# Performance work log

Hardware: AMD Instinct MI355X
Metric: run time of the kernel (lower is better)

Reference implementation:

```python
import jax, jax.numpy as jnp
import numpy as np

B, TIN, IN, TRI, D, FFN, L, OUT = 8, 1040, 80, 128, 512, 2048, 8, 1024
H, DH, STRIDE, SEG, RC, LC, MAXMEM = 8, 64, 4, 16, 4, 32, 4
NEG = -1e8
SCALE = DH ** -0.5


def _layer_norm(x, g, b, eps=1e-5):
    m = jnp.mean(x, -1, keepdims=True)
    v = jnp.var(x, -1, keepdims=True)
    return (x - m) * jax.lax.rsqrt(v + eps) * g + b


def _build_attention_mask(U, nseg):
    # Faithful port of Emformer._gen_attention_mask; True = masked out.
    rct = RC * nseg
    mlen = nseg - 1
    rc_rows, q_rows, s_rows = [], [], []
    for i in range(nseg):
        rs, re = i * RC, i * RC + RC
        ss, se = max(i * SEG - LC, 0), min((i + 1) * SEG, U)
        ms = max(i - MAXMEM, 0)
        widths = [ms, i - ms, mlen - i, rs, RC, rct - re, ss, se - ss, U - se]

        def row(allowed):
            return np.concatenate([np.full(max(w, 0), j in allowed, dtype=bool)
                                   for j, w in enumerate(widths)])

        r = row({1, 4, 7})  # memory, own rc block, own (left-extended) segment
        rc_rows.append(np.tile(r, (RC, 1)))
        q_rows.append(np.tile(r, (min(SEG, U - i * SEG), 1)))
        s_rows.append(row({4, 7})[None])  # summary: rc block + segment only
    allow = np.concatenate([np.concatenate(rc_rows), np.concatenate(q_rows), np.concatenate(s_rows)])
    return jnp.asarray(~allow)


def _forward(input, lengths, w_in, ln_in_g, ln_in_b, wq, bq, wk, bk, wv, bv, wo, bo,
             ff_ln_g, ff_ln_b, w1, b1, w2, b2, ln_out_g, ln_out_b, w_out, b_out, lng, lnb):
    x = input @ w_in                                    # (B, TIN, TRI) input_linear (no bias)
    nb, t, _ = x.shape
    nf = t - t % STRIDE
    x = x[:, :nf].reshape(nb, nf // STRIDE, TRI * STRIDE)  # time reduction -> (B, Tr, D)
    lr = lengths // STRIDE
    x = jnp.transpose(x, (1, 0, 2))                     # (Tr, B, D) time-major like torch Emformer
    Tr = x.shape[0]
    U = Tr - RC                                         # utterance length (256)
    nseg = -(-U // SEG)
    utt = x[:U]
    # right-context blocks: hard-copied per segment (last block = trailing rc)
    starts = np.concatenate([np.arange(1, nseg) * SEG, [Tr - RC]])
    idx = (starts[:, None] + np.arange(RC)[None, :]).reshape(-1)
    rc = x[idx]                                         # (nseg*RC, B, D)
    Rt = rc.shape[0]
    Q = Rt + U + nseg                                   # rc + utterance + summary queries
    K = (nseg - 1) + Rt + U                             # mems + rc + utterance keys
    attn_mask = _build_attention_mask(U, nseg)          # (Q, K)
    mems0 = utt.reshape(nseg, SEG, nb, D).mean(1)[:-1]  # AvgPool1d(seg) on raw utterance, drop last
    # padding mask over keys (faithful to _gen_padding_mask)
    rcbl = Q - jnp.max(lr) - nseg
    klen = lr + (nseg - 1) + rcbl
    pad = jnp.arange(K)[None, :] >= klen[:, None]       # (B, K), True = masked

    def step(carry, p):
        utt, rc, mems = carry
        g1, be1, Wq, Bq, Wk, Bk, Wv, Bv, Wo, Bo, g2, be2, Wf1, Bf1, Wf2, Bf2, g3, be3 = p
        ln = _layer_norm(jnp.concatenate([rc, utt]), g1, be1)
        ln_rc, ln_utt = ln[:Rt], ln[Rt:]
        summary = ln_utt.reshape(nseg, SEG, nb, D).mean(1)       # (nseg, B, D)
        qin = jnp.concatenate([ln_rc, ln_utt, summary])          # (Q, B, D)
        kin = jnp.concatenate([mems, ln_rc, ln_utt])             # (K, B, D)
        q = (qin @ Wq + Bq).reshape(Q, nb, H, DH)
        k = (kin @ Wk + Bk).reshape(K, nb, H, DH)
        v = (kin @ Wv + Bv).reshape(K, nb, H, DH)
        w = jnp.einsum('qbhd,kbhd->bhqk', q * SCALE, k)
        w = jnp.where(attn_mask[None, None], NEG, w)
        w = jnp.where(pad[:, None, None, :], NEG, w)
        probs = jax.nn.softmax(w, axis=-1)
        att = jnp.einsum('bhqk,kbhd->qbhd', probs, v).reshape(Q, nb, D)
        out = att @ Wo + Bo
        rcu = out[:Rt + U]
        new_mems = jnp.tanh(out[Rt + U:])[:-1]                   # tanh_on_mem=True, drop last summary
        res = rcu + jnp.concatenate([rc, utt])                   # residual w/ pre-LN input
        h = _layer_norm(res, g2, be2)
        h = jax.nn.relu(h @ Wf1 + Bf1) @ Wf2 + Bf2               # pos_ff (pre-LN inside)
        res = res + h
        res = _layer_norm(res, g3, be3)
        return (res[Rt:], res[:Rt], new_mems), None

    xs = (ln_in_g, ln_in_b, wq, bq, wk, bk, wv, bv, wo, bo,
          ff_ln_g, ff_ln_b, w1, b1, w2, b2, ln_out_g, ln_out_b)
    (utt, rc, mems), _ = jax.lax.scan(step, (utt, rc, mems0), xs)
    y = jnp.transpose(utt, (1, 0, 2))                   # (B, U, D)
    y = _layer_norm(y @ w_out + b_out, lng, lnb)        # output_linear + LayerNorm
    return y, lr


def setup_inputs() -> dict:
    key = jax.random.key(0)
    ks = jax.random.split(key, 12)

    def w(k, shape, fan):
        return jax.random.normal(k, shape, jnp.float32) / np.sqrt(fan)

    return {
        "input": jax.random.normal(ks[0], (B, TIN, IN), jnp.float32),
        "lengths": jax.random.randint(ks[1], (B,), 256, 1025, jnp.int32),
        "w_in": w(ks[2], (IN, TRI), IN),
        "ln_in_g": jnp.ones((L, D), jnp.float32), "ln_in_b": jnp.zeros((L, D), jnp.float32),
        "wq": w(ks[3], (L, D, D), D), "bq": jnp.zeros((L, D), jnp.float32),
        "wk": w(ks[4], (L, D, D), D), "bk": jnp.zeros((L, D), jnp.float32),
        "wv": w(ks[5], (L, D, D), D), "bv": jnp.zeros((L, D), jnp.float32),
        "wo": w(ks[6], (L, D, D), D), "bo": jnp.zeros((L, D), jnp.float32),
        "ff_ln_g": jnp.ones((L, D), jnp.float32), "ff_ln_b": jnp.zeros((L, D), jnp.float32),
        "w1": w(ks[7], (L, D, FFN), D), "b1": jnp.zeros((L, FFN), jnp.float32),
        "w2": w(ks[8], (L, FFN, D), FFN), "b2": jnp.zeros((L, D), jnp.float32),
        "ln_out_g": jnp.ones((L, D), jnp.float32), "ln_out_b": jnp.zeros((L, D), jnp.float32),
        "w_out": w(ks[9], (D, OUT), D), "b_out": jnp.zeros((OUT,), jnp.float32),
        "lng": jnp.ones((OUT,), jnp.float32), "lnb": jnp.zeros((OUT,), jnp.float32),
    }


def reference(input, lengths, w_in, ln_in_g, ln_in_b, wq, bq, wk, bk, wv, bv, wo, bo,
              ff_ln_g, ff_ln_b, w1, b1, w2, b2, ln_out_g, ln_out_b, w_out, b_out, lng, lnb):
    return _forward(input, lengths, w_in, ln_in_g, ln_in_b, wq, bq, wk, bk, wv, bv, wo, bo,
                    ff_ln_g, ff_ln_b, w1, b1, w2, b2, ln_out_g, ln_out_b, w_out, b_out, lng, lnb)
```

## Files before the change

### kernel.cpp

```cpp
#include <hip/hip_runtime.h>
#include <math.h>

#define NB 8
#define D 512
#define H 8
#define DH 64
#define NSEG 16
#define RT 64
#define UU 256
#define QN 336
#define KN 335
#define SROWS 320
#define FFN_D 2048
#define LAYERS 8
#define OUTD 1024
#define TR 260
#define NEGV (-100000000.0f)
#define QSCALE 0.125f

typedef __attribute__((ext_vector_type(8))) short bf16x8;
typedef __attribute__((ext_vector_type(4))) float f32x4;

__device__ inline unsigned short f2bf(float f) {
    union { float f; unsigned int u; } v; v.f = f;
    unsigned int u = v.u;
    unsigned int r = (u + 0x7FFFu + ((u >> 16) & 1u)) >> 16;
    return (unsigned short)r;
}
__device__ inline float bf2f(unsigned short h) {
    union { unsigned int u; float f; } v; v.u = ((unsigned int)h) << 16;
    return v.f;
}

__device__ inline void async16(const void* g, void* l) {
    __builtin_amdgcn_global_load_lds((const __attribute__((address_space(1))) void*)g,
                                     (__attribute__((address_space(3))) void*)l, 16, 0, 0);
}

__global__ void lr_k(const int* __restrict__ lengths, int* __restrict__ lrw,
                     float* __restrict__ out_lr) {
    if (threadIdx.x == 0) {
        int mx = 0;
        for (int b = 0; b < NB; ++b) {
            int v = lengths[b] >> 2;
            lrw[b] = v;
            out_lr[b] = (float)v;
            if (v > mx) mx = v;
        }
        lrw[NB] = mx;
    }
}

__global__ __launch_bounds__(128) void inproj_k(const float* __restrict__ input,
                                                const float* __restrict__ w_in,
                                                float* __restrict__ XB) {
    __shared__ float wl[80 * 128];
    __shared__ float il[4 * 80];
    int tid = threadIdx.x;
    int t = blockIdx.x >> 3;
    int b = blockIdx.x & 7;
    for (int i = tid; i < 80 * 128; i += 128) wl[i] = w_in[i];
    const float* inp = input + ((size_t)b * 1040 + (size_t)t * 4) * 80;
    for (int i = tid; i < 320; i += 128) il[i] = inp[i];
    __syncthreads();
    float* xrow = XB + ((size_t)(t * NB + b)) * D;
#pragma unroll
    for (int c = 0; c < 4; ++c) {
        float acc = 0.f;
        for (int i = 0; i < 80; ++i) acc = fmaf(il[c * 80 + i], wl[i * 128 + tid], acc);
        xrow[c * 128 + tid] = acc;
    }
}

__global__ __launch_bounds__(256) void initstate_k(const float* __restrict__ XB,
                                                   float* __restrict__ S) {
    int r = blockIdx.x;
    int srow = r >> 3, b = r & 7;
    int src;
    if (srow < RT) {
        int i = srow >> 2, jj = srow & 3;
        src = (i < 15 ? (i + 1) * 16 : 256) + jj;
    } else {
        src = srow - RT;
    }
    const float* xr = XB + ((size_t)(src * NB + b)) * D;
    float* sr = S + (size_t)r * D;
    sr[threadIdx.x] = xr[threadIdx.x];
    sr[threadIdx.x + 256] = xr[threadIdx.x + 256];
}

__global__ __launch_bounds__(256) void mems0_k(const float* __restrict__ XB,
                                               unsigned short* __restrict__ MEMS) {
    int ib = blockIdx.x;
    int i = ib >> 3, b = ib & 7;
    for (int c = 0; c < 2; ++c) {
        int col = threadIdx.x + c * 256;
        float s = 0.f;
#pragma unroll
        for (int t = 0; t < 16; ++t) s += XB[((size_t)((i * 16 + t) * NB + b)) * D + col];
        MEMS[(size_t)ib * D + col] = f2bf(s * (1.f / 16.f));
    }
}

__global__ __launch_bounds__(256) void ln2_k(float* __restrict__ X,
                                             unsigned short* __restrict__ Y16,
                                             const float* __restrict__ gA,
                                             const float* __restrict__ bA,
                                             const float* __restrict__ gB,
                                             const float* __restrict__ bB, int fused) {
    int row = blockIdx.x;
    float* x = X + (size_t)row * D;
    __shared__ float rs_[4], rss_[4], rs2[4], rss2[4];
    int w = threadIdx.x >> 6;
    float v[2];
    float s = 0.f, ss = 0.f;
#pragma unroll
    for (int j = 0; j < 2; ++j) {
        v[j] = x[threadIdx.x + j * 256];
        s += v[j];
        ss = fmaf(v[j], v[j], ss);
    }
#pragma unroll
    for (int off = 32; off; off >>= 1) {
        s += __shfl_xor(s, off);
        ss += __shfl_xor(ss, off);
    }
    if ((threadIdx.x & 63) == 0) { rs_[w] = s; rss_[w] = ss; }
    __syncthreads();
    s = rs_[0] + rs_[1] + rs_[2] + rs_[3];
    ss = rss_[0] + rss_[1] + rss_[2] + rss_[3];
    float mean = s * (1.f / D);
    float var = ss * (1.f / D) - mean * mean;
    float rstd = rsqrtf(var + 1e-5f);
    float y1[2];
#pragma unroll
    for (int j = 0; j < 2; ++j) {
        int col = threadIdx.x + j * 256;
        y1[j] = (v[j] - mean) * rstd * gA[col] + bA[col];
    }
    if (!fused) {
#pragma unroll
        for (int j = 0; j < 2; ++j)
            Y16[(size_t)row * D + threadIdx.x + j * 256] = f2bf(y1[j]);
        return;
    }
    float s2 = 0.f, ss2 = 0.f;
#pragma unroll
    for (int j = 0; j < 2; ++j) {
        s2 += y1[j];
        ss2 = fmaf(y1[j], y1[j], ss2);
    }
#pragma unroll
    for (int off = 32; off; off >>= 1) {
        s2 += __shfl_xor(s2, off);
        ss2 += __shfl_xor(ss2, off);
    }
    if ((threadIdx.x & 63) == 0) { rs2[w] = s2; rss2[w] = ss2; }
    __syncthreads();
    s2 = rs2[0] + rs2[1] + rs2[2] + rs2[3];
    ss2 = rss2[0] + rss2[1] + rss2[2] + rss2[3];
    float mean2 = s2 * (1.f / D);
    float var2 = ss2 * (1.f / D) - mean2 * mean2;
    float rstd2 = rsqrtf(var2 + 1e-5f);
#pragma unroll
    for (int j = 0; j < 2; ++j) {
        int col = threadIdx.x + j * 256;
        x[col] = y1[j];
        Y16[(size_t)row * D + col] = f2bf((y1[j] - mean2) * rstd2 * gB[col] + bB[col]);
    }
}

__global__ __launch_bounds__(256) void ln_res_k(const float* __restrict__ OUTB,
                                                float* __restrict__ SB,
                                                unsigned short* __restrict__ MEMS,
                                                unsigned short* __restrict__ Y16,
                                                const float* __restrict__ g,
                                                const float* __restrict__ be) {
    int row = blockIdx.x;
    if (row >= SROWS * NB) {
        int j = row - SROWS * NB;
#pragma unroll
        for (int c = 0; c < 2; ++c) {
            int col = threadIdx.x + c * 256;
            MEMS[(size_t)j * D + col] = f2bf(tanhf(OUTB[(size_t)row * D + col]));
        }
        return;
    }
    float v[2];
    float s = 0.f, ss = 0.f;
#pragma unroll
    for (int j = 0; j < 2; ++j) {
        int col = threadIdx.x + j * 256;
        float r = SB[(size_t)row * D + col] + OUTB[(size_t)row * D + col];
        SB[(size_t)row * D + col] = r;
        v[j] = r;
        s += r;
        ss = fmaf(r, r, ss);
    }
#pragma unroll
    for (int off = 32; off; off >>= 1) {
        s += __shfl_xor(s, off);
        ss += __shfl_xor(ss, off);
    }
    __shared__ float rs_[4], rss_[4];
    int w = threadIdx.x >> 6;
    if ((threadIdx.x & 63) == 0) {
        rs_[w] = s;
        rss_[w] = ss;
    }
    __syncthreads();
    s = rs_[0] + rs_[1] + rs_[2] + rs_[3];
    ss = rss_[0] + rss_[1] + rss_[2] + rss_[3];
    float mean = s * (1.f / D);
    float var = ss * (1.f / D) - mean * mean;
    float rstd = rsqrtf(var + 1e-5f);
#pragma unroll
    for (int j = 0; j < 2; ++j) {
        int col = threadIdx.x + j * 256;
        Y16[(size_t)row * D + col] = f2bf((v[j] - mean) * rstd * g[col] + be[col]);
    }
}

__device__ inline void conv_tile64(float (*tile)[65], const float* __restrict__ src, int srcN,
                                   int k0, int sn0, unsigned short* __restrict__ dst, int dstK,
                                   int dn0) {
    int t = threadIdx.x;
#pragma unroll
    for (int p = 0; p < 4; ++p) {
        int r = p * 16 + (t >> 4);
        int c = (t & 15) * 4;
        *(float4*)&tile[r][c] = *(const float4*)&src[(size_t)(k0 + r) * srcN + sn0 + c];
    }
    __syncthreads();
#pragma unroll
    for (int p = 0; p < 2; ++p) {
        int rn = p * 32 + (t >> 3);
        int kc = (t & 7) * 8;
        int4 o;
        o.x = (int)f2bf(tile[kc + 0][rn]) | ((int)f2bf(tile[kc + 1][rn]) << 16);
        o.y = (int)f2bf(tile[kc + 2][rn]) | ((int)f2bf(tile[kc + 3][rn]) << 16);
        o.z = (int)f2bf(tile[kc + 4][rn]) | ((int)f2bf(tile[kc + 5][rn]) << 16);
        o.w = (int)f2bf(tile[kc + 6][rn]) | ((int)f2bf(tile[kc + 7][rn]) << 16);
        *(int4*)&dst[(size_t)(dn0 + rn) * dstK + k0 + kc] = o;
    }
    __syncthreads();
}

__global__ __launch_bounds__(256) void convw_all_k(const float* __restrict__ wq,
                                                   const float* __restrict__ wk,
                                                   const float* __restrict__ wv,
                                                   const float* __restrict__ wo,
                                                   const float* __restrict__ w1,
                                                   const float* __restrict__ w2,
                                                   const float* __restrict__ bq,
                                                   const float* __restrict__ bk,
                                                   const float* __restrict__ bv,
                                                   const float* __restrict__ w_out,
                                                   unsigned short* __restrict__ WQKV,
                                                   unsigned short* __restrict__ WO16,
                                                   unsigned short* __restrict__ W1T,
                                                   unsigned short* __restrict__ W2T,
                                                   unsigned short* __restrict__ WOUT16,
                                                   float* __restrict__ BQKV) {
    __shared__ float tile[64][65];
    int tb = blockIdx.x;
    if (tb >= LAYERS * 768) {
        int t = tb - LAYERS * 768;
        int n0 = (t % 16) * 64, k0 = (t / 16) * 64;
        conv_tile64(tile, w_out, 1024, k0, n0, WOUT16, 512, n0);
        return;
    }
    int l = tb / 768, t = tb % 768;
    if (t == 0) {
        for (int i = threadIdx.x; i < 1536; i += 256)
            BQKV[l * 1536 + i] = i < 512 ? bq[l * 512 + i]
                                         : (i < 1024 ? bk[l * 512 + i - 512]
                                                     : bv[l * 512 + i - 1024]);
    }
    if (t < 192) {
        int n0 = (t % 24) * 64, k0 = (t / 24) * 64;
        const float* src;
        int sn0;
        if (n0 < 512) { src = wq + (size_t)l * 262144; sn0 = n0; }
        else if (n0 < 1024) { src = wk + (size_t)l * 262144; sn0 = n0 - 512; }
        else { src = wv + (size_t)l * 262144; sn0 = n0 - 1024; }
        conv_tile64(tile, src, 512, k0, sn0, WQKV + (size_t)l * 1536 * 512, 512, n0);
    } else if (t < 256) {
        int tt = t - 192;
        int n0 = (tt % 8) * 64, k0 = (tt / 8) * 64;
        conv_tile64(tile, wo + (size_t)l * 262144, 512, k0, n0, WO16 + (size_t)l * 512 * 512, 512,
                    n0);
    } else if (t < 512) {
        int tt = t - 256;
        int n0 = (tt % 32) * 64, k0 = (tt / 32) * 64;
        conv_tile64(tile, w1 + (size_t)l * 1048576, 2048, k0, n0, W1T + (size_t)l * 2048 * 512,
                    512, n0);
    } else {
        int tt = t - 512;
        int n0 = (tt % 8) * 64, k0 = (tt / 8) * 64;
        conv_tile64(tile, w2 + (size_t)l * 1048576, 512, k0, n0, W2T + (size_t)l * 512 * 2048,
                    2048, n0);
    }
}

__global__ __launch_bounds__(256) void gemm16_k(const unsigned short* __restrict__ A,
                                                const unsigned short* __restrict__ BT,
                                                const float* __restrict__ bias,
                                                void* __restrict__ Cp, int M, int N, int K,
                                                int Kchunk, int flags) {
    __shared__ unsigned short As[2 * 64 * 64];
    __shared__ unsigned short Bs[2 * 64 * 64];
    int tid = threadIdx.x;
    int wave = tid >> 6, lane = tid & 63;
    int wm = wave >> 1, wn = wave & 1;
    int quad = lane >> 4, sub = lane & 15;
    int m0 = blockIdx.y * 64, n0 = blockIdx.x * 64;
    int kb = blockIdx.z * Kchunk;

    int s0 = wave * 128 + lane;
    int s1 = s0 + 64;
    int r0 = s0 >> 3, c0 = (s0 & 7) ^ (r0 & 7);
    int r1 = s1 >> 3, c1 = (s1 & 7) ^ (r1 & 7);
    int gra0 = m0 + r0; if (gra0 >= M) gra0 = M - 1;
    int gra1 = m0 + r1; if (gra1 >= M) gra1 = M - 1;
    const unsigned short* gA0 = A + (size_t)gra0 * K + kb + c0 * 8;
    const unsigned short* gA1 = A + (size_t)gra1 * K + kb + c1 * 8;
    const unsigned short* gB0 = BT + (size_t)(n0 + r0) * K + kb + c0 * 8;
    const unsigned short* gB1 = BT + (size_t)(n0 + r1) * K + kb + c1 * 8;
    int lo0 = (wave * 128) * 8;
    int lo1 = (wave * 128 + 64) * 8;

    int rowA0 = wm * 32 + sub, rowA1 = rowA0 + 16;
    int rowB0 = wn * 32 + sub, rowB1 = rowB0 + 16;

    int nIter = Kchunk >> 6;
    f32x4 acc[2][2] = {};

    async16(gA0, &As[lo0]);
    async16(gA1, &As[lo1]);
    async16(gB0, &Bs[lo0]);
    async16(gB1, &Bs[lo1]);

    for (int it = 0; it < nIter; ++it) {
        __syncthreads();
        int bo = (it & 1) * 4096;
        if (it + 1 < nIter) {
            int nb = ((it + 1) & 1) * 4096;
            int ko = (it + 1) * 64;
            async16(gA0 + ko, &As[nb + lo0]);
            async16(gA1 + ko, &As[nb + lo1]);
            async16(gB0 + ko, &Bs[nb + lo0]);
            async16(gB1 + ko, &Bs[nb + lo1]);
        }
#pragma unroll
        for (int ks = 0; ks < 2; ++ks) {
            int cc = ks * 4 + quad;
            bf16x8 af0 = *(const bf16x8*)&As[bo + rowA0 * 64 + ((cc ^ (rowA0 & 7)) * 8)];
            bf16x8 af1 = *(const bf16x8*)&As[bo + rowA1 * 64 + ((cc ^ (rowA1 & 7)) * 8)];
            bf16x8 bf0 = *(const bf16x8*)&Bs[bo + rowB0 * 64 + ((cc ^ (rowB0 & 7)) * 8)];
            bf16x8 bf1 = *(const bf16x8*)&Bs[bo + rowB1 * 64 + ((cc ^ (rowB1 & 7)) * 8)];
            acc[0][0] = __builtin_amdgcn_mfma_f32_16x16x32_bf16(af0, bf0, acc[0][0], 0, 0, 0);
            acc[0][1] = __builtin_amdgcn_mfma_f32_16x16x32_bf16(af0, bf1, acc[0][1], 0, 0, 0);
            acc[1][0] = __builtin_amdgcn_mfma_f32_16x16x32_bf16(af1, bf0, acc[1][0], 0, 0, 0);
            acc[1][1] = __builtin_amdgcn_mfma_f32_16x16x32_bf16(af1, bf1, acc[1][1], 0, 0, 0);
        }
    }

    bool relu = flags & 1, addc = flags & 2, obf = flags & 4, atom = flags & 8;
    bool addbias = !atom || blockIdx.z == 0;
    float* Cf = (float*)Cp;
    unsigned short* Ch = (unsigned short*)Cp;
#pragma unroll
    for (int mi = 0; mi < 2; ++mi) {
#pragma unroll
        for (int ni = 0; ni < 2; ++ni) {
#pragma unroll
            for (int r = 0; r < 4; ++r) {
                int row = m0 + wm * 32 + mi * 16 + quad * 4 + r;
                int col = n0 + wn * 32 + ni * 16 + sub;
                if (row < M) {
                    float v = acc[mi][ni][r] + (addbias ? bias[col] : 0.f);
                    if (relu) v = fmaxf(v, 0.f);
                    size_t idx = (size_t)row * N + col;
                    if (obf) {
                        Ch[idx] = f2bf(v);
                    } else if (atom) {
                        atomicAdd(&Cf[idx], v);
                    } else {
                        if (addc) v += Cf[idx];
                        Cf[idx] = v;
                    }
                }
            }
        }
    }
}

__global__ __launch_bounds__(256) void attn_k(const unsigned short* __restrict__ QKV,
                                              unsigned short* __restrict__ ATT,
                                              const int* __restrict__ lrw) {
    int tid = threadIdx.x;
    int qrow = blockIdx.x;
    int b = blockIdx.y;

    int i, is_sum;
    if (qrow < RT) {
        i = qrow >> 2;
        is_sum = 0;
    } else if (qrow < RT + UU) {
        i = (qrow - RT) >> 4;
        is_sum = 0;
    } else {
        i = qrow - (RT + UU);
        is_sum = 1;
    }
    int ms = (i > 4) ? (i - 4) : 0;
    int n_mem = is_sum ? 0 : (i - ms);
    int us = (i * 16 - 32 > 0) ? (i * 16 - 32) : 0;
    int ue = (i + 1) * 16;
    int total = n_mem + 4 + (ue - us);
    int klen = KN + lrw[b] - lrw[NB];

    __shared__ float qs[512];
    __shared__ float sc[H][64];
    __shared__ int kks[64];

    if (!is_sum) {
        const unsigned int* qrp =
            (const unsigned int*)&QKV[(size_t)(120 + qrow * NB + b) * 1536];
        unsigned int u = qrp[tid];
        qs[2 * tid] = __uint_as_float(u << 16) * QSCALE;
        qs[2 * tid + 1] = __uint_as_float(u & 0xFFFF0000u) * QSCALE;
    } else {
        const unsigned int* qrp =
            (const unsigned int*)&QKV[(size_t)(120 + (RT + i * 16) * NB + b) * 1536];
        float a0 = 0.f, a1 = 0.f;
#pragma unroll
        for (int t = 0; t < 16; ++t) {
            unsigned int u = qrp[(size_t)t * (NB * 768) + tid];
            a0 += __uint_as_float(u << 16);
            a1 += __uint_as_float(u & 0xFFFF0000u);
        }
        qs[2 * tid] = a0 * (QSCALE / 16.f);
        qs[2 * tid + 1] = a1 * (QSCALE / 16.f);
    }
    if (tid < 64) {
        int kk = -1;
        if (tid < total) {
            if (tid < n_mem)
                kk = ms + tid;
            else if (tid < n_mem + 4)
                kk = 15 + i * 4 + (tid - n_mem);
            else
                kk = 79 + us + (tid - n_mem - 4);
        }
        kks[tid] = kk;
    }
    __syncthreads();

#pragma unroll
    for (int rep = 0; rep < 2; ++rep) {
        int p = rep * 256 + tid;
        int h = p >> 6, j = p & 63;
        int kk = kks[j];
        float s = NEGV;
        if (kk >= 0 && kk < klen) {
            const int4* kr = (const int4*)&QKV[(size_t)(kk * NB + b) * 1536 + 512 + h * DH];
            const float* qh = &qs[h * DH];
            float accd = 0.f;
#pragma unroll
            for (int c = 0; c < 8; ++c) {
                int4 kv = kr[c];
                const int uu[4] = {kv.x, kv.y, kv.z, kv.w};
#pragma unroll
                for (int jj = 0; jj < 4; ++jj) {
                    float lo = __uint_as_float(((unsigned)uu[jj]) << 16);
                    float hi = __uint_as_float(((unsigned)uu[jj]) & 0xFFFF0000u);
                    accd = fmaf(lo, qh[c * 8 + jj * 2], accd);
                    accd = fmaf(hi, qh[c * 8 + jj * 2 + 1], accd);
                }
            }
            s = accd;
        }
        sc[h][j] = s;
    }
    __syncthreads();

    {
        int wv = tid >> 6, lane = tid & 63;
#pragma unroll
        for (int hh = 0; hh < 2; ++hh) {
            int h = wv + hh * 4;
            float s = sc[h][lane];
            float m = s;
#pragma unroll
            for (int off = 32; off; off >>= 1) m = fmaxf(m, __shfl_xor(m, off));
            float p = __expf(s - m);
            float sum = p;
#pragma unroll
            for (int off = 32; off; off >>= 1) sum += __shfl_xor(sum, off);
            sc[h][lane] = p / sum;
        }
    }
    __syncthreads();

    {
        int h = tid >> 5;
        const float* ph = sc[h];
        float a0 = 0.f, a1 = 0.f;
        const unsigned short* vbase = QKV + (size_t)b * 1536 + 1024 + 2 * tid;
#pragma unroll 4
        for (int j = 0; j < total; ++j) {
            int kkj = kks[j];
            unsigned int u = *(const unsigned int*)&vbase[(size_t)kkj * (NB * 1536)];
            float p = ph[j];
            a0 = fmaf(p, __uint_as_float(u << 16), a0);
            a1 = fmaf(p, __uint_as_float(u & 0xFFFF0000u), a1);
        }
        unsigned int o = ((unsigned int)f2bf(a0)) | (((unsigned int)f2bf(a1)) << 16);
        *(unsigned int*)&ATT[(size_t)(qrow * NB + b) * D + 2 * tid] = o;
    }
}

__global__ __launch_bounds__(256) void final_ln_k(const float* __restrict__ Yb,
                                                  const float* __restrict__ g,
                                                  const float* __restrict__ be,
                                                  float* __restrict__ out) {
    int row = blockIdx.x;
    int u = row >> 3, b = row & 7;
    const float* x = Yb + (size_t)row * OUTD;
    float v[4];
    float s = 0.f, ss = 0.f;
#pragma unroll
    for (int j = 0; j < 4; ++j) {
        v[j] = x[threadIdx.x + j * 256];
        s += v[j];
        ss = fmaf(v[j], v[j], ss);
    }
#pragma unroll
    for (int off = 32; off; off >>= 1) {
        s += __shfl_xor(s, off);
        ss += __shfl_xor(ss, off);
    }
    __shared__ float rs_[4], rss_[4];
    int w = threadIdx.x >> 6;
    if ((threadIdx.x & 63) == 0) {
        rs_[w] = s;
        rss_[w] = ss;
    }
    __syncthreads();
    s = rs_[0] + rs_[1] + rs_[2] + rs_[3];
    ss = rss_[0] + rss_[1] + rss_[2] + rss_[3];
    float mean = s * (1.f / OUTD);
    float var = ss * (1.f / OUTD) - mean * mean;
    float rstd = rsqrtf(var + 1e-5f);
    float* o = out + ((size_t)(b * 256 + u)) * OUTD;
#pragma unroll
    for (int j = 0; j < 4; ++j) {
        int col = threadIdx.x + j * 256;
        o[col] = (v[j] - mean) * rstd * g[col] + be[col];
    }
}

extern "C" void kernel_launch(void* const* d_in, const int* in_sizes, int n_in, void* d_out,
                              int out_size, void* d_ws, size_t ws_size, hipStream_t stream) {
    (void)in_sizes;
    (void)n_in;
    (void)out_size;
    (void)ws_size;
    const float* input = (const float*)d_in[0];
    const int* lengths = (const int*)d_in[1];
    const float* w_in = (const float*)d_in[2];
    const float* ln_in_g = (const float*)d_in[3];
    const float* ln_in_b = (const float*)d_in[4];
    const float* wq = (const float*)d_in[5];
    const float* bq = (const float*)d_in[6];
    const float* wk = (const float*)d_in[7];
    const float* bk = (const float*)d_in[8];
    const float* wv = (const float*)d_in[9];
    const float* bv = (const float*)d_in[10];
    const float* wo = (const float*)d_in[11];
    const float* bo = (const float*)d_in[12];
    const float* ff_g = (const float*)d_in[13];
    const float* ff_b = (const float*)d_in[14];
    const float* w1 = (const float*)d_in[15];
    const float* b1 = (const float*)d_in[16];
    const float* w2 = (const float*)d_in[17];
    const float* b2 = (const float*)d_in[18];
    const float* lo_g = (const float*)d_in[19];
    const float* lo_b = (const float*)d_in[20];
    const float* w_out = (const float*)d_in[21];
    const float* b_out = (const float*)d_in[22];
    const float* lng = (const float*)d_in[23];
    const float* lnb = (const float*)d_in[24];
    float* out = (float*)d_out;

    char* wsc = (char*)d_ws;
    size_t off = 0;
    auto alloc = [&](size_t bytes) {
        char* p = wsc + off;
        off += (bytes + 255) & ~(size_t)255;
        return p;
    };
    unsigned short* ACT16 = (unsigned short*)alloc(2688ULL * 512 * 2);
    unsigned short* ATT16 = (unsigned short*)alloc(2688ULL * 512 * 2);
    unsigned short* HB16 = (unsigned short*)alloc(2560ULL * 2048 * 2);
    unsigned short* QKVB = (unsigned short*)alloc(2688ULL * 1536 * 2);
    float* SB = (float*)alloc(2560ULL * 512 * 4);
    unsigned short* WQKV16 = (unsigned short*)alloc(8ULL * 1536 * 512 * 2);
    unsigned short* WO16 = (unsigned short*)alloc(8ULL * 512 * 512 * 2);
    unsigned short* W1T = (unsigned short*)alloc(8ULL * 2048 * 512 * 2);
    unsigned short* W2T = (unsigned short*)alloc(8ULL * 512 * 2048 * 2);
    unsigned short* WOUT16 = (unsigned short*)alloc(1024ULL * 512 * 2);
    float* BQKV = (float*)alloc(8ULL * 1536 * 4);
    int* LRW = (int*)alloc(64);

    unsigned short* MEMS16 = ACT16;
    unsigned short* LNB16 = ACT16 + 120 * 512;
    float* XB = (float*)QKVB;
    float* OUTB = (float*)QKVB;
    float* HBf = (float*)QKVB;

    lr_k<<<1, 64, 0, stream>>>(lengths, LRW, out + (size_t)NB * 256 * 1024);
    convw_all_k<<<LAYERS * 768 + 128, 256, 0, stream>>>(wq, wk, wv, wo, w1, w2, bq, bk, bv,
                                                        w_out, WQKV16, WO16, W1T, W2T, WOUT16,
                                                        BQKV);
    inproj_k<<<TR * NB, 128, 0, stream>>>(input, w_in, XB);
    initstate_k<<<SROWS * NB, 256, 0, stream>>>(XB, SB);
    mems0_k<<<15 * NB, 256, 0, stream>>>(XB, MEMS16);

    for (int l = 0; l < LAYERS; ++l) {
        if (l == 0) {
            ln2_k<<<SROWS * NB, 256, 0, stream>>>(SB, LNB16, ln_in_g, ln_in_b, nullptr, nullptr,
                                                  0);
        } else {
            ln2_k<<<SROWS * NB, 256, 0, stream>>>(SB, LNB16, lo_g + (l - 1) * D,
                                                  lo_b + (l - 1) * D, ln_in_g + l * D,
                                                  ln_in_b + l * D, 1);
        }
        gemm16_k<<<dim3(24, 42, 1), 256, 0, stream>>>(ACT16, WQKV16 + (size_t)l * 1536 * 512,
                                                      BQKV + l * 1536, QKVB, 2680, 1536, 512,
                                                      512, 4);
        attn_k<<<dim3(QN, NB), 256, 0, stream>>>(QKVB, ATT16, LRW);
        gemm16_k<<<dim3(8, 42, 1), 256, 0, stream>>>(ATT16, WO16 + (size_t)l * 512 * 512,
                                                     bo + l * D, OUTB, QN * NB, D, D, 512, 0);
        ln_res_k<<<(SROWS + 15) * NB, 256, 0, stream>>>(OUTB, SB, MEMS16, LNB16, ff_g + l * D,
                                                        ff_b + l * D);
        gemm16_k<<<dim3(32, 40, 1), 256, 0, stream>>>(LNB16, W1T + (size_t)l * 2048 * 512,
                                                      b1 + l * FFN_D, HB16, SROWS * NB, FFN_D,
                                                      512, 512, 1 | 4);
        gemm16_k<<<dim3(8, 40, 4), 256, 0, stream>>>(HB16, W2T + (size_t)l * 512 * 2048,
                                                     b2 + l * D, SB, SROWS * NB, D, FFN_D, 512,
                                                     8);
    }
    ln2_k<<<SROWS * NB, 256, 0, stream>>>(SB, LNB16, lo_g + 7 * D, lo_b + 7 * D, nullptr,
                                          nullptr, 0);
    gemm16_k<<<dim3(16, 32, 1), 256, 0, stream>>>(LNB16 + (size_t)RT * NB * D, WOUT16, b_out,
                                                  HBf, UU * NB, OUTD, 512, 512, 0);
    final_ln_k<<<UU * NB, 256, 0, stream>>>(HBf, lng, lnb, out);
}
```

Measured before the change: 1.176 ms.

## Merge setup kernels and drop GEMM LDS double buffering

Folds the lengths kernel into the weight-conversion launch as one extra block, and merges the initial-state copy and the memory-average kernels into a single launch, removing two kernel launches. The GEMM also goes from double-buffered to single-buffered LDS, issuing its async loads at the top of each K step with a barrier before and after compute. This halves the GEMM's shared memory, which may allow more resident blocks, but it gives up the overlap between the next tile's loads and the current MFMAs.

```diff
diff --git a/kernel.cpp b/kernel.cpp
--- a/kernel.cpp
+++ b/kernel.cpp
@@ -37,20 +37,6 @@
                                      (__attribute__((address_space(3))) void*)l, 16, 0, 0);
 }
 
-__global__ void lr_k(const int* __restrict__ lengths, int* __restrict__ lrw,
-                     float* __restrict__ out_lr) {
-    if (threadIdx.x == 0) {
-        int mx = 0;
-        for (int b = 0; b < NB; ++b) {
-            int v = lengths[b] >> 2;
-            lrw[b] = v;
-            out_lr[b] = (float)v;
-            if (v > mx) mx = v;
-        }
-        lrw[NB] = mx;
-    }
-}
-
 __global__ __launch_bounds__(128) void inproj_k(const float* __restrict__ input,
                                                 const float* __restrict__ w_in,
                                                 float* __restrict__ XB) {
@@ -72,26 +58,26 @@
     }
 }
 
-__global__ __launch_bounds__(256) void initstate_k(const float* __restrict__ XB,
-                                                   float* __restrict__ S) {
+__global__ __launch_bounds__(256) void init2_k(const float* __restrict__ XB,
+                                               float* __restrict__ S,
+                                               unsigned short* __restrict__ MEMS) {
     int r = blockIdx.x;
-    int srow = r >> 3, b = r & 7;
-    int src;
-    if (srow < RT) {
-        int i = srow >> 2, jj = srow & 3;
-        src = (i < 15 ? (i + 1) * 16 : 256) + jj;
-    } else {
-        src = srow - RT;
-    }
-    const float* xr = XB + ((size_t)(src * NB + b)) * D;
-    float* sr = S + (size_t)r * D;
-    sr[threadIdx.x] = xr[threadIdx.x];
-    sr[threadIdx.x + 256] = xr[threadIdx.x + 256];
-}
-
-__global__ __launch_bounds__(256) void mems0_k(const float* __restrict__ XB,
-                                               unsigned short* __restrict__ MEMS) {
-    int ib = blockIdx.x;
+    if (r < SROWS * NB) {
+        int srow = r >> 3, b = r & 7;
+        int src;
+        if (srow < RT) {
+            int i = srow >> 2, jj = srow & 3;
+            src = (i < 15 ? (i + 1) * 16 : 256) + jj;
+        } else {
+            src = srow - RT;
+        }
+        const float* xr = XB + ((size_t)(src * NB + b)) * D;
+        float* sr = S + (size_t)r * D;
+        sr[threadIdx.x] = xr[threadIdx.x];
+        sr[threadIdx.x + 256] = xr[threadIdx.x + 256];
+        return;
+    }
+    int ib = r - SROWS * NB;
     int i = ib >> 3, b = ib & 7;
     for (int c = 0; c < 2; ++c) {
         int col = threadIdx.x + c * 256;
@@ -261,9 +247,25 @@
                                                    unsigned short* __restrict__ W1T,
                                                    unsigned short* __restrict__ W2T,
                                                    unsigned short* __restrict__ WOUT16,
-                                                   float* __restrict__ BQKV) {
+                                                   float* __restrict__ BQKV,
+                                                   const int* __restrict__ lengths,
+                                                   int* __restrict__ lrw,
+                                                   float* __restrict__ out_lr) {
     __shared__ float tile[64][65];
     int tb = blockIdx.x;
+    if (tb >= LAYERS * 768 + 128) {
+        if (threadIdx.x == 0) {
+            int mx = 0;
+            for (int b = 0; b < NB; ++b) {
+                int v = lengths[b] >> 2;
+                lrw[b] = v;
+                out_lr[b] = (float)v;
+                if (v > mx) mx = v;
+            }
+            lrw[NB] = mx;
+        }
+        return;
+    }
     if (tb >= LAYERS * 768) {
         int t = tb - LAYERS * 768;
         int n0 = (t % 16) * 64, k0 = (t / 16) * 64;
@@ -308,8 +310,8 @@
                                                 const float* __restrict__ bias,
                                                 void* __restrict__ Cp, int M, int N, int K,
                                                 int Kchunk, int flags) {
-    __shared__ unsigned short As[2 * 64 * 64];
-    __shared__ unsigned short Bs[2 * 64 * 64];
+    __shared__ unsigned short As[64 * 64];
+    __shared__ unsigned short Bs[64 * 64];
     int tid = threadIdx.x;
     int wave = tid >> 6, lane = tid & 63;
     int wm = wave >> 1, wn = wave & 1;
@@ -327,43 +329,34 @@
     const unsigned short* gA1 = A + (size_t)gra1 * K + kb + c1 * 8;
     const unsigned short* gB0 = BT + (size_t)(n0 + r0) * K + kb + c0 * 8;
     const unsigned short* gB1 = BT + (size_t)(n0 + r1) * K + kb + c1 * 8;
-    int lo0 = (wave * 128) * 8;
-    int lo1 = (wave * 128 + 64) * 8;
+    unsigned short* lA0 = &As[(wave * 128) * 8];
+    unsigned short* lA1 = &As[(wave * 128 + 64) * 8];
+    unsigned short* lB0 = &Bs[(wave * 128) * 8];
+    unsigned short* lB1 = &Bs[(wave * 128 + 64) * 8];
 
     int rowA0 = wm * 32 + sub, rowA1 = rowA0 + 16;
     int rowB0 = wn * 32 + sub, rowB1 = rowB0 + 16;
 
-    int nIter = Kchunk >> 6;
     f32x4 acc[2][2] = {};
-
-    async16(gA0, &As[lo0]);
-    async16(gA1, &As[lo1]);
-    async16(gB0, &Bs[lo0]);
-    async16(gB1, &Bs[lo1]);
-
-    for (int it = 0; it < nIter; ++it) {
+    for (int k0 = 0; k0 < Kchunk; k0 += 64) {
+        async16(gA0 + k0, lA0);
+        async16(gA1 + k0, lA1);
+        async16(gB0 + k0, lB0);
+        async16(gB1 + k0, lB1);
         __syncthreads();
-        int bo = (it & 1) * 4096;
-        if (it + 1 < nIter) {
-            int nb = ((it + 1) & 1) * 4096;
-            int ko = (it + 1) * 64;
-            async16(gA0 + ko, &As[nb + lo0]);
-            async16(gA1 + ko, &As[nb + lo1]);
-            async16(gB0 + ko, &Bs[nb + lo0]);
-            async16(gB1 + ko, &Bs[nb + lo1]);
-        }
 #pragma unroll
         for (int ks = 0; ks < 2; ++ks) {
             int cc = ks * 4 + quad;
-            bf16x8 af0 = *(const bf16x8*)&As[bo + rowA0 * 64 + ((cc ^ (rowA0 & 7)) * 8)];
-            bf16x8 af1 = *(const bf16x8*)&As[bo + rowA1 * 64 + ((cc ^ (rowA1 & 7)) * 8)];
-            bf16x8 bf0 = *(const bf16x8*)&Bs[bo + rowB0 * 64 + ((cc ^ (rowB0 & 7)) * 8)];
-            bf16x8 bf1 = *(const bf16x8*)&Bs[bo + rowB1 * 64 + ((cc ^ (rowB1 & 7)) * 8)];
+            bf16x8 af0 = *(const bf16x8*)&As[rowA0 * 64 + ((cc ^ (rowA0 & 7)) * 8)];
+            bf16x8 af1 = *(const bf16x8*)&As[rowA1 * 64 + ((cc ^ (rowA1 & 7)) * 8)];
+            bf16x8 bf0 = *(const bf16x8*)&Bs[rowB0 * 64 + ((cc ^ (rowB0 & 7)) * 8)];
+            bf16x8 bf1 = *(const bf16x8*)&Bs[rowB1 * 64 + ((cc ^ (rowB1 & 7)) * 8)];
             acc[0][0] = __builtin_amdgcn_mfma_f32_16x16x32_bf16(af0, bf0, acc[0][0], 0, 0, 0);
             acc[0][1] = __builtin_amdgcn_mfma_f32_16x16x32_bf16(af0, bf1, acc[0][1], 0, 0, 0);
             acc[1][0] = __builtin_amdgcn_mfma_f32_16x16x32_bf16(af1, bf0, acc[1][0], 0, 0, 0);
             acc[1][1] = __builtin_amdgcn_mfma_f32_16x16x32_bf16(af1, bf1, acc[1][1], 0, 0, 0);
         }
+        __syncthreads();
     }
 
     bool relu = flags & 1, addc = flags & 2, obf = flags & 4, atom = flags & 8;
@@ -621,13 +614,11 @@
     float* OUTB = (float*)QKVB;
     float* HBf = (float*)QKVB;
 
-    lr_k<<<1, 64, 0, stream>>>(lengths, LRW, out + (size_t)NB * 256 * 1024);
-    convw_all_k<<<LAYERS * 768 + 128, 256, 0, stream>>>(wq, wk, wv, wo, w1, w2, bq, bk, bv,
-                                                        w_out, WQKV16, WO16, W1T, W2T, WOUT16,
-                                                        BQKV);
+    convw_all_k<<<LAYERS * 768 + 129, 256, 0, stream>>>(
+        wq, wk, wv, wo, w1, w2, bq, bk, bv, w_out, WQKV16, WO16, W1T, W2T, WOUT16, BQKV, lengths,
+        LRW, out + (size_t)NB * 256 * 1024);
     inproj_k<<<TR * NB, 128, 0, stream>>>(input, w_in, XB);
-    initstate_k<<<SROWS * NB, 256, 0, stream>>>(XB, SB);
-    mems0_k<<<15 * NB, 256, 0, stream>>>(XB, MEMS16);
+    init2_k<<<(SROWS + 15) * NB, 256, 0, stream>>>(XB, SB, MEMS16);
 
     for (int l = 0; l < LAYERS; ++l) {
         if (l == 0) {
```

Result: faster. 1.076 ms (-8.5%).
